# Optimization experiments

Hardware: AMD Instinct MI355X
Metric: run time of the kernel (lower is better)

## Reference

```python
import jax, jax.numpy as jnp
import numpy as np

N_KERNELS = 11

def _kernel_mus(n):
    l = [1.0]
    if n == 1:
        return l
    b = 2.0 / (n - 1)
    l.append(1 - b / 2)
    for i in range(1, n - 1):
        l.append(l[i] - b)
    return l

def _kernel_sigmas(n):
    b = 2.0 / (n - 1)
    l = [0.0001]
    if n == 1:
        return l
    l += [0.5 * b] * (n - 1)
    return l

MU = jnp.asarray(np.array(_kernel_mus(N_KERNELS), dtype=np.float32))      # [K]
SIGMA = jnp.asarray(np.array(_kernel_sigmas(N_KERNELS), dtype=np.float32))  # [K]


def setup_inputs() -> dict:
    key = jax.random.key(0)
    k1, k2, k3, k4 = jax.random.split(key, 4)
    B, Q, D, V, E = 256, 32, 512, 100000, 300
    return {
        "query_tokens": jax.random.randint(k1, (B, Q), 0, V),
        "doc_tokens": jax.random.randint(k2, (B, D), 0, V),
        "emb": jax.random.normal(k3, (V, E), dtype=jnp.float32),
        "fc_w": jax.random.normal(k4, (1, N_KERNELS), dtype=jnp.float32),
        "fc_b": jnp.zeros((1,), dtype=jnp.float32),
    }


def reference(query_tokens, doc_tokens, emb, fc_w, fc_b):
    q_mask = (query_tokens > 0).astype(jnp.float32)  # [B,Q]
    d_mask = (doc_tokens > 0).astype(jnp.float32)    # [B,D]

    qe = emb[query_tokens]  # [B,Q,E]
    de = emb[doc_tokens]    # [B,D,E]

    # Cosine match matrix (CosineMatrixAttention: L2-normalize with tiny eps)
    qn = qe / (jnp.linalg.norm(qe, axis=-1, keepdims=True) + 1e-13)
    dn = de / (jnp.linalg.norm(de, axis=-1, keepdims=True) + 1e-13)
    mm = jnp.einsum("bqe,bde->bqd", qn, dn)  # [B,Q,D]

    mask = q_mask[:, :, None] * d_mask[:, None, :]  # [B,Q,D]
    mm = mm * mask

    # Gaussian RBF kernel pooling: [B,Q,D,K]
    diff = mm[..., None] - MU[None, None, None, :]
    rbf = jnp.exp(-jnp.square(diff) / (2.0 * jnp.square(SIGMA)[None, None, None, :]))
    rbf = rbf * mask[..., None]

    query_kernels = rbf.sum(axis=2)  # [B,Q,K]
    log_qk = jnp.log(jnp.maximum(query_kernels, 1e-10)) * 0.01
    # NOTE: original code computes a masked version but (bug) sums the UNMASKED
    # log_query_kernels; we faithfully replicate that.
    kernels = log_qk.sum(axis=1)  # [B,K]

    score = kernels @ fc_w.T + fc_b  # [B,1]
    return score
```

## Files before the change

kernel.cpp:

```cpp
#include <hip/hip_runtime.h>
#include <hip/hip_bf16.h>
#include <math.h>


#define NB 256
#define NQ 32
#define ND 512
#define NE 300
#define NF4 75
#define LROW 328
#define SPLITS 2
#define DPB 256
#define CHUNK 64
#define NCHUNK 4
#define NT 512
#define NK 11
#define QK_SZ (NQ * NK)
#define PART_BYTES (NB * SPLITS * QK_SZ * 4)

typedef __bf16 bf16x8 __attribute__((ext_vector_type(8)));
typedef __bf16 bf16x4 __attribute__((ext_vector_type(4)));
typedef float f32x4 __attribute__((ext_vector_type(4)));

__global__ __launch_bounds__(NT, 4) void knrm_main(
    const int* __restrict__ qtok,
    const int* __restrict__ dtok,
    const float* __restrict__ emb,
    const float* __restrict__ fcw,
    const float* __restrict__ fcb,
    float* __restrict__ partial,
    int* __restrict__ done_cnt,
    float* __restrict__ out)
{
  __shared__ __align__(16) __bf16 qlds[NQ][LROW];
  __shared__ __align__(16) __bf16 dlds[CHUNK][LROW];
  __shared__ float qscale[NQ];
  __shared__ float dscale[CHUNK];
  __shared__ float qkl[QK_SZ];
  __shared__ int last_flag;

  const int b    = blockIdx.x >> 1;
  const int sp   = blockIdx.x & 1;
  const int t    = threadIdx.x;
  const int lane = t & 63;
  const int w    = t >> 6;

  const int dr = t >> 3;
  const int dj = t & 7;
  int td4[NCHUNK];
  #pragma unroll
  for (int ch = 0; ch < NCHUNK; ++ch)
    td4[ch] = dtok[b * ND + sp * DPB + ch * CHUNK + dr];

  float4 v[10];
  {
    const float4* rowp = (const float4*)(emb + (size_t)td4[0] * NE);
    #pragma unroll
    for (int i = 0; i < 9; ++i) v[i] = rowp[dj + 8 * i];
    v[9] = (dj < 3) ? rowp[dj + 72] : make_float4(0.f, 0.f, 0.f, 0.f);
  }

  if (t < QK_SZ && (t % NK) != 0) qkl[t] = 0.0f;

  {
    const int r = t >> 4;
    const int j = t & 15;
    const int tq = qtok[b * NQ + r];
    const float4* rowp = (const float4*)(emb + (size_t)tq * NE);

    float4 qv[5];
    #pragma unroll
    for (int i = 0; i < 4; ++i) qv[i] = rowp[j + 16 * i];
    qv[4] = (j < 11) ? rowp[j + 64] : make_float4(0.f, 0.f, 0.f, 0.f);

    float ss = 0.0f;
    #pragma unroll
    for (int i = 0; i < 5; ++i) {
      ss += qv[i].x * qv[i].x + qv[i].y * qv[i].y + qv[i].z * qv[i].z + qv[i].w * qv[i].w;
      if (i < 4 || j < 11) {
        bf16x4 h;
        h[0] = (__bf16)qv[i].x; h[1] = (__bf16)qv[i].y;
        h[2] = (__bf16)qv[i].z; h[3] = (__bf16)qv[i].w;
        *(bf16x4*)&qlds[r][4 * (j + 16 * i)] = h;
      }
    }
    if (j < 5) { bf16x4 z = {}; *(bf16x4*)&qlds[r][NE + 4 * j] = z; }
    ss += __shfl_xor(ss, 1, 16);
    ss += __shfl_xor(ss, 2, 16);
    ss += __shfl_xor(ss, 4, 16);
    ss += __shfl_xor(ss, 8, 16);
    if (j == 0) qscale[r] = (tq > 0) ? 1.0f / (sqrtf(ss) + 1e-13f) : 0.0f;

    int cnt = 0;
    #pragma unroll
    for (int jj = 0; jj < DPB / 16; ++jj) {
      int td = dtok[b * ND + sp * DPB + j + 16 * jj];
      cnt += (tq > 0 && td == tq) ? 1 : 0;
    }
    cnt += __shfl_xor(cnt, 1, 16);
    cnt += __shfl_xor(cnt, 2, 16);
    cnt += __shfl_xor(cnt, 4, 16);
    cnt += __shfl_xor(cnt, 8, 16);
    if (j == 0) qkl[r * NK] = (float)cnt;
  }
  __syncthreads();

  const int mt  = w >> 2;
  const int nt  = w & 3;
  const int l15 = lane & 15;
  const int l4  = lane >> 4;

  float rbfacc[4][10];
  #pragma unroll
  for (int r4 = 0; r4 < 4; ++r4)
    #pragma unroll
    for (int k = 0; k < 10; ++k) rbfacc[r4][k] = 0.0f;

  const __bf16* aptr = &qlds[mt * 16 + l15][l4 * 8];
  const __bf16* bptr = &dlds[nt * 16 + l15][l4 * 8];

  float qs[4];
  #pragma unroll
  for (int r4 = 0; r4 < 4; ++r4) qs[r4] = qscale[mt * 16 + l4 * 4 + r4];

  const float muk[10] = {0.9f, 0.7f, 0.5f, 0.3f, 0.1f,
                         -0.1f, -0.3f, -0.5f, -0.7f, -0.9f};

  #pragma unroll 1
  for (int ch = 0; ch < NCHUNK; ++ch) {
    {
      float ss = 0.0f;
      #pragma unroll
      for (int i = 0; i < 10; ++i) {
        ss += v[i].x * v[i].x + v[i].y * v[i].y + v[i].z * v[i].z + v[i].w * v[i].w;
        if (i < 9 || dj < 3) {
          bf16x4 h;
          h[0] = (__bf16)v[i].x; h[1] = (__bf16)v[i].y;
          h[2] = (__bf16)v[i].z; h[3] = (__bf16)v[i].w;
          *(bf16x4*)&dlds[dr][4 * (dj + 8 * i)] = h;
        }
      }
      if (dj < 5) { bf16x4 z = {}; *(bf16x4*)&dlds[dr][NE + 4 * dj] = z; }
      ss += __shfl_xor(ss, 1, 8);
      ss += __shfl_xor(ss, 2, 8);
      ss += __shfl_xor(ss, 4, 8);
      if (dj == 0) dscale[dr] = (td4[ch] > 0) ? 1.0f / (sqrtf(ss) + 1e-13f) : 0.0f;
    }
    __syncthreads();

    {
      const int chn = (ch + 1) & (NCHUNK - 1);
      const float4* rowp = (const float4*)(emb + (size_t)td4[chn] * NE);
      #pragma unroll
      for (int i = 0; i < 9; ++i) v[i] = rowp[dj + 8 * i];
      v[9] = (dj < 3) ? rowp[dj + 72] : make_float4(0.f, 0.f, 0.f, 0.f);
    }

    f32x4 acc = {};
    #pragma unroll
    for (int k = 0; k < 10; ++k) {
      bf16x8 av = *(const bf16x8*)(aptr + k * 32);
      bf16x8 bv = *(const bf16x8*)(bptr + k * 32);
      acc = __builtin_amdgcn_mfma_f32_16x16x32_bf16(av, bv, acc, 0, 0, 0);
    }

    const float ds = dscale[nt * 16 + l15];
    #pragma unroll
    for (int r4 = 0; r4 < 4; ++r4) {
      const float s = qs[r4] * ds;
      const float mm = (s == 0.0f) ? 1e8f : acc[r4] * s;
      #pragma unroll
      for (int k = 0; k < 10; ++k) {
        float d = mm - muk[k];
        rbfacc[r4][k] += __builtin_amdgcn_exp2f(d * d * -72.13475204444817f);
      }
    }
    __syncthreads();
  }

  #pragma unroll
  for (int r4 = 0; r4 < 4; ++r4)
    #pragma unroll
    for (int k = 0; k < 10; ++k) {
      float vv = rbfacc[r4][k];
      vv += __shfl_xor(vv, 1);
      vv += __shfl_xor(vv, 2);
      vv += __shfl_xor(vv, 4);
      vv += __shfl_xor(vv, 8);
      if (l15 == 0) atomicAdd(&qkl[(mt * 16 + l4 * 4 + r4) * NK + k + 1], vv);
    }
  __syncthreads();

  float* pp = partial + ((size_t)b * SPLITS + sp) * QK_SZ;
  for (int i = t; i < QK_SZ; i += NT) pp[i] = qkl[i];
  __syncthreads();

  if (t == 0) {
    __threadfence();
    int old = atomicAdd(&done_cnt[b], 1);
    last_flag = (old == 1);
  }
  __syncthreads();
  if (last_flag && w == 0) {
    __threadfence();
    const float* po = partial + ((size_t)b * SPLITS + (sp ^ 1)) * QK_SZ;
    float acc = 0.0f;
    for (int i = lane; i < QK_SZ; i += 64) {
      float s = qkl[i] + po[i];
      acc += logf(fmaxf(s, 1e-10f)) * 0.01f * fcw[i % NK];
    }
    #pragma unroll
    for (int off = 1; off < 64; off <<= 1) acc += __shfl_xor(acc, off);
    if (lane == 0) out[b] = acc + fcb[0];
  }
}

extern "C" void kernel_launch(void* const* d_in, const int* in_sizes, int n_in,
                              void* d_out, int out_size, void* d_ws, size_t ws_size,
                              hipStream_t stream) {
  const int* qtok = (const int*)d_in[0];
  const int* dtok = (const int*)d_in[1];
  const float* emb = (const float*)d_in[2];
  const float* fcw = (const float*)d_in[3];
  const float* fcb = (const float*)d_in[4];
  float* out = (float*)d_out;
  float* partial = (float*)d_ws;
  int* done_cnt = (int*)((char*)d_ws + PART_BYTES);

  hipMemsetAsync(done_cnt, 0, NB * sizeof(int), stream);
  knrm_main<<<NB * SPLITS, NT, 0, stream>>>(qtok, dtok, emb, fcw, fcb,
                                            partial, done_cnt, out);
}
```

Measured before the change: 216.8 us.

## Drop register prefetch of doc embeddings and load each chunk in-loop with wider stores

Removes the register-held prefetch of the next document chunk's embedding rows, so each chunk's rows are now loaded at the top of its loop iteration. Each thread handles pairs of float4s and writes bf16x8 to LDS instead of bf16x4. The barrier placement moves: the post-query-staging sync and the end-of-iteration sync are replaced by one sync at the loop start. qscale is re-read from LDS inside the loop. This lowers register pressure, which may help occupancy, but it loses the overlap of global loads with MFMA and exp work.

```diff
diff --git a/kernel.cpp b/kernel.cpp
--- a/kernel.cpp
+++ b/kernel.cpp
@@ -47,18 +47,11 @@
 
   const int dr = t >> 3;
   const int dj = t & 7;
+
   int td4[NCHUNK];
   #pragma unroll
   for (int ch = 0; ch < NCHUNK; ++ch)
     td4[ch] = dtok[b * ND + sp * DPB + ch * CHUNK + dr];
-
-  float4 v[10];
-  {
-    const float4* rowp = (const float4*)(emb + (size_t)td4[0] * NE);
-    #pragma unroll
-    for (int i = 0; i < 9; ++i) v[i] = rowp[dj + 8 * i];
-    v[9] = (dj < 3) ? rowp[dj + 72] : make_float4(0.f, 0.f, 0.f, 0.f);
-  }
 
   if (t < QK_SZ && (t % NK) != 0) qkl[t] = 0.0f;
 
@@ -103,7 +96,6 @@
     cnt += __shfl_xor(cnt, 8, 16);
     if (j == 0) qkl[r * NK] = (float)cnt;
   }
-  __syncthreads();
 
   const int mt  = w >> 2;
   const int nt  = w & 3;
@@ -119,42 +111,51 @@
   const __bf16* aptr = &qlds[mt * 16 + l15][l4 * 8];
   const __bf16* bptr = &dlds[nt * 16 + l15][l4 * 8];
 
-  float qs[4];
-  #pragma unroll
-  for (int r4 = 0; r4 < 4; ++r4) qs[r4] = qscale[mt * 16 + l4 * 4 + r4];
-
   const float muk[10] = {0.9f, 0.7f, 0.5f, 0.3f, 0.1f,
                          -0.1f, -0.3f, -0.5f, -0.7f, -0.9f};
 
   #pragma unroll 1
   for (int ch = 0; ch < NCHUNK; ++ch) {
+    __syncthreads();
     {
+      const int td = td4[ch];
+      const float4* rowp = (const float4*)(emb + (size_t)td * NE);
+
+      float4 va[5][2];
+      #pragma unroll
+      for (int i = 0; i < 4; ++i) {
+        va[i][0] = rowp[2 * dj + 16 * i];
+        va[i][1] = rowp[2 * dj + 16 * i + 1];
+      }
+      va[4][0] = (dj <= 5) ? rowp[64 + 2 * dj] : make_float4(0.f, 0.f, 0.f, 0.f);
+      va[4][1] = (dj <= 4) ? rowp[65 + 2 * dj] : make_float4(0.f, 0.f, 0.f, 0.f);
+
       float ss = 0.0f;
       #pragma unroll
-      for (int i = 0; i < 10; ++i) {
-        ss += v[i].x * v[i].x + v[i].y * v[i].y + v[i].z * v[i].z + v[i].w * v[i].w;
-        if (i < 9 || dj < 3) {
-          bf16x4 h;
-          h[0] = (__bf16)v[i].x; h[1] = (__bf16)v[i].y;
-          h[2] = (__bf16)v[i].z; h[3] = (__bf16)v[i].w;
-          *(bf16x4*)&dlds[dr][4 * (dj + 8 * i)] = h;
+      for (int i = 0; i < 5; ++i) {
+        ss += va[i][0].x * va[i][0].x + va[i][0].y * va[i][0].y
+            + va[i][0].z * va[i][0].z + va[i][0].w * va[i][0].w;
+        ss += va[i][1].x * va[i][1].x + va[i][1].y * va[i][1].y
+            + va[i][1].z * va[i][1].z + va[i][1].w * va[i][1].w;
+        bf16x8 h;
+        h[0] = (__bf16)va[i][0].x; h[1] = (__bf16)va[i][0].y;
+        h[2] = (__bf16)va[i][0].z; h[3] = (__bf16)va[i][0].w;
+        h[4] = (__bf16)va[i][1].x; h[5] = (__bf16)va[i][1].y;
+        h[6] = (__bf16)va[i][1].z; h[7] = (__bf16)va[i][1].w;
+        if (i < 4 || dj <= 4) {
+          *(bf16x8*)&dlds[dr][8 * dj + 64 * i] = h;
+        } else if (dj == 5) {
+          bf16x4 h4; h4[0] = h[0]; h4[1] = h[1]; h4[2] = h[2]; h4[3] = h[3];
+          *(bf16x4*)&dlds[dr][8 * dj + 64 * i] = h4;
         }
       }
       if (dj < 5) { bf16x4 z = {}; *(bf16x4*)&dlds[dr][NE + 4 * dj] = z; }
       ss += __shfl_xor(ss, 1, 8);
       ss += __shfl_xor(ss, 2, 8);
       ss += __shfl_xor(ss, 4, 8);
-      if (dj == 0) dscale[dr] = (td4[ch] > 0) ? 1.0f / (sqrtf(ss) + 1e-13f) : 0.0f;
+      if (dj == 0) dscale[dr] = (td > 0) ? 1.0f / (sqrtf(ss) + 1e-13f) : 0.0f;
     }
     __syncthreads();
-
-    {
-      const int chn = (ch + 1) & (NCHUNK - 1);
-      const float4* rowp = (const float4*)(emb + (size_t)td4[chn] * NE);
-      #pragma unroll
-      for (int i = 0; i < 9; ++i) v[i] = rowp[dj + 8 * i];
-      v[9] = (dj < 3) ? rowp[dj + 72] : make_float4(0.f, 0.f, 0.f, 0.f);
-    }
 
     f32x4 acc = {};
     #pragma unroll
@@ -167,7 +168,8 @@
     const float ds = dscale[nt * 16 + l15];
     #pragma unroll
     for (int r4 = 0; r4 < 4; ++r4) {
-      const float s = qs[r4] * ds;
+      const float qs = qscale[mt * 16 + l4 * 4 + r4];
+      const float s = qs * ds;
       const float mm = (s == 0.0f) ? 1e8f : acc[r4] * s;
       #pragma unroll
       for (int k = 0; k < 10; ++k) {
@@ -175,7 +177,6 @@
         rbfacc[r4][k] += __builtin_amdgcn_exp2f(d * d * -72.13475204444817f);
       }
     }
-    __syncthreads();
   }
 
   #pragma unroll
```

Result: no change. 213.8 us (-1.4%).
